# Performance work log

Measured on AMD Instinct MI355X. Metric: run time of the kernel, lower is better.

Reference implementation:

```python
import jax, jax.numpy as jnp
import numpy as np

N = 100000
D_FEAT = 256
HID = 128
EMB = 64
FANOUT = 16


def setup_inputs() -> dict:
    key = jax.random.key(0)
    k = jax.random.split(key, 7)
    s = 0.05
    features = jax.random.normal(k[0], (N, D_FEAT), dtype=jnp.float32)
    W1 = jax.random.normal(k[1], (HID, 2 * D_FEAT), dtype=jnp.float32) * s
    W2 = jax.random.normal(k[2], (HID, 2 * HID), dtype=jnp.float32) * s
    W3 = jax.random.normal(k[3], (HID, 2 * HID), dtype=jnp.float32) * s
    W4 = jax.random.normal(k[4], (EMB, 2 * HID), dtype=jnp.float32) * s
    nodes = jnp.arange(N, dtype=jnp.int32)
    neigh = jax.random.randint(k[5], (N, FANOUT), 0, N, dtype=jnp.int32)
    return {"features": features, "W1": W1, "W2": W2, "W3": W3, "W4": W4,
            "nodes": nodes, "neigh": neigh}


def _sage_layer(h, neigh, W):
    # MeanAggregator: mean of sampled neighbor features  [N, d]
    neigh_mean = jnp.mean(h[neigh], axis=1)
    # Encoder (gcn=False): relu(W @ cat([self, neigh_mean]).T) -> [N, out]
    combined = jnp.concatenate([h, neigh_mean], axis=1)  # [N, 2d]
    return jax.nn.relu(combined @ W.T)


def reference(features, W1, W2, W3, W4, nodes, neigh):
    h1 = _sage_layer(features, neigh, W1)  # [N, HID]
    h2 = _sage_layer(h1, neigh, W2)        # [N, HID]
    h3 = _sage_layer(h2, neigh, W3)        # [N, HID]
    h4 = _sage_layer(h3, neigh, W4)        # [N, EMB]
    # GraphEmbeddingModule.forward returns gSAGE4(n).t() -> [len(n), EMB]
    return h4[nodes]
```

## Files before the change

### kernel.cpp

```cpp
#include <hip/hip_runtime.h>
#include <hip/hip_bf16.h>


constexpr int N_NODES = 100000;
constexpr int FANOUT  = 16;

typedef __attribute__((ext_vector_type(8))) short short8;
typedef __attribute__((ext_vector_type(4))) float f32x4;

__device__ inline unsigned short bf16_rne(float f) {
    unsigned u = __float_as_uint(f);
    return (unsigned short)((u + 0x7fffu + ((u >> 16) & 1u)) >> 16);
}
__device__ inline float bf16_tof(unsigned short s) {
    return __uint_as_float(((unsigned)s) << 16);
}

__global__ __launch_bounds__(256)
void prep_Bck(const float* __restrict__ W, unsigned short* __restrict__ Bhi,
              unsigned short* __restrict__ Blo, int D_IN, int D_OUT)
{
    int i = blockIdx.x * 256 + threadIdx.x;
    int total = 2 * D_OUT * D_IN;
    if (i >= total) return;
    int c = i / D_IN, k = i % D_IN;
    float v = (c < D_OUT) ? W[(size_t)c * (2 * D_IN) + k]
                          : W[(size_t)(c - D_OUT) * (2 * D_IN) + D_IN + k];
    unsigned short hi = bf16_rne(v);
    Bhi[i] = hi;
    Blo[i] = bf16_rne(v - bf16_tof(hi));
}

__global__ __launch_bounds__(256, 4)
void gemm1(const float* __restrict__ hf,
           const unsigned short* __restrict__ Bhi,
           const unsigned short* __restrict__ Blo,
           float* __restrict__ gs, unsigned short* __restrict__ gn, int N)
{
    constexpr int K = 256, DO = 128, LDA = 40;
    __shared__ unsigned short Ah[64 * LDA], Al[64 * LDA];

    const int tid  = threadIdx.x;
    const int wave = tid >> 6;
    const int lane = tid & 63;
    const int ml   = lane & 15;
    const int quad = lane >> 4;
    const int node0 = blockIdx.x * 64;

    f32x4 acc[4][4];
    #pragma unroll
    for (int mi = 0; mi < 4; ++mi)
        #pragma unroll
        for (int ni = 0; ni < 4; ++ni)
            acc[mi][ni] = (f32x4){0.f, 0.f, 0.f, 0.f};

    for (int k0 = 0; k0 < K; k0 += 32) {
        #pragma unroll
        for (int t = 0; t < 2; ++t) {
            int idx = tid + t * 256;
            int row = idx >> 3, c4 = idx & 7;
            int nd = node0 + row; if (nd >= N) nd = N - 1;
            float4 v = *(const float4*)&hf[(size_t)nd * K + k0 + c4 * 4];
            float vv[4] = {v.x, v.y, v.z, v.w};
            unsigned short hi[4], lo[4];
            #pragma unroll
            for (int e = 0; e < 4; ++e) {
                hi[e] = bf16_rne(vv[e]);
                lo[e] = bf16_rne(vv[e] - bf16_tof(hi[e]));
            }
            *(uint2*)&Ah[row * LDA + c4 * 4] = *(const uint2*)hi;
            *(uint2*)&Al[row * LDA + c4 * 4] = *(const uint2*)lo;
        }
        __syncthreads();

        short8 afh[4], afl[4];
        #pragma unroll
        for (int mi = 0; mi < 4; ++mi) {
            int r = mi * 16 + ml;
            afh[mi] = *(const short8*)&Ah[r * LDA + quad * 8];
            afl[mi] = *(const short8*)&Al[r * LDA + quad * 8];
        }
        #pragma unroll
        for (int ni = 0; ni < 4; ++ni) {
            int c = wave * 64 + ni * 16 + ml;
            short8 bh = *(const short8*)&Bhi[(size_t)c * K + k0 + quad * 8];
            short8 bl = *(const short8*)&Blo[(size_t)c * K + k0 + quad * 8];
            #pragma unroll
            for (int mi = 0; mi < 4; ++mi) {
                acc[mi][ni] = __builtin_amdgcn_mfma_f32_16x16x32_bf16(afl[mi], bh, acc[mi][ni], 0, 0, 0);
                acc[mi][ni] = __builtin_amdgcn_mfma_f32_16x16x32_bf16(afh[mi], bl, acc[mi][ni], 0, 0, 0);
                acc[mi][ni] = __builtin_amdgcn_mfma_f32_16x16x32_bf16(afh[mi], bh, acc[mi][ni], 0, 0, 0);
            }
        }
        __syncthreads();
    }

    #pragma unroll
    for (int mi = 0; mi < 4; ++mi)
        #pragma unroll
        for (int r = 0; r < 4; ++r) {
            int node = node0 + mi * 16 + quad * 4 + r;
            if (node >= N) continue;
            #pragma unroll
            for (int ni = 0; ni < 4; ++ni) {
                int c = wave * 64 + ni * 16 + ml;
                float v = acc[mi][ni][r];
                if (c < DO) gs[(size_t)node * DO + c] = v;
                else        gn[(size_t)node * DO + (c - DO)] = bf16_rne(v);
            }
        }
}

template<int C>
__global__ __launch_bounds__(256, 4)
void fused_layer(const float* __restrict__ gs_in,
                 const unsigned short* __restrict__ gn_in,
                 const int* __restrict__ neigh,
                 const unsigned short* __restrict__ Bhi,
                 const unsigned short* __restrict__ Blo,
                 float* __restrict__ gs_out,
                 unsigned short* __restrict__ gn_out, int N)
{
    constexpr int K = 128, DO = C / 2, NI = C / 64, LDAF = 136;
    __shared__ unsigned short Afh[64 * LDAF], Afl[64 * LDAF];

    const int tid  = threadIdx.x;
    const int wave = tid >> 6;
    const int lane = tid & 63;
    const int ml   = lane & 15;
    const int quad = lane >> 4;
    const int node0 = blockIdx.x * 64;

    {
        const int row = tid >> 2;
        const int seg = tid & 3;
        int nd = node0 + row; if (nd >= N) nd = N - 1;
        const int4* nb4 = (const int4*)(neigh + (size_t)nd * FANOUT);
        int4 q0 = nb4[0], q1 = nb4[1], q2 = nb4[2], q3 = nb4[3];
        int ids[FANOUT] = {q0.x, q0.y, q0.z, q0.w, q1.x, q1.y, q1.z, q1.w,
                           q2.x, q2.y, q2.z, q2.w, q3.x, q3.y, q3.z, q3.w};
        float acc[32];
        #pragma unroll
        for (int c = 0; c < 32; ++c) acc[c] = 0.f;
        #pragma unroll
        for (int j = 0; j < FANOUT; ++j) {
            const uint4* src = (const uint4*)&gn_in[(size_t)ids[j] * 128 + seg * 32];
            #pragma unroll
            for (int t = 0; t < 4; ++t) {
                uint4 q = src[t];
                acc[t*8+0] += __uint_as_float(q.x << 16);
                acc[t*8+1] += __uint_as_float(q.x & 0xffff0000u);
                acc[t*8+2] += __uint_as_float(q.y << 16);
                acc[t*8+3] += __uint_as_float(q.y & 0xffff0000u);
                acc[t*8+4] += __uint_as_float(q.z << 16);
                acc[t*8+5] += __uint_as_float(q.z & 0xffff0000u);
                acc[t*8+6] += __uint_as_float(q.w << 16);
                acc[t*8+7] += __uint_as_float(q.w & 0xffff0000u);
            }
        }
        const float inv = 1.0f / (float)FANOUT;
        alignas(16) unsigned short th[32], tl[32];
        const float4* gsp = (const float4*)&gs_in[(size_t)nd * 128 + seg * 32];
        #pragma unroll
        for (int t = 0; t < 8; ++t) {
            float4 s = gsp[t];
            float sv[4] = {s.x, s.y, s.z, s.w};
            #pragma unroll
            for (int e = 0; e < 4; ++e) {
                float h = fmaxf(fmaf(acc[t*4+e], inv, sv[e]), 0.f);
                unsigned short hi = bf16_rne(h);
                th[t*4+e] = hi;
                tl[t*4+e] = bf16_rne(h - bf16_tof(hi));
            }
        }
        #pragma unroll
        for (int t = 0; t < 4; ++t) {
            *(uint4*)&Afh[row * LDAF + seg * 32 + t * 8] = *(const uint4*)&th[t * 8];
            *(uint4*)&Afl[row * LDAF + seg * 32 + t * 8] = *(const uint4*)&tl[t * 8];
        }
    }
    __syncthreads();

    f32x4 acc[4][NI];
    #pragma unroll
    for (int mi = 0; mi < 4; ++mi)
        #pragma unroll
        for (int ni = 0; ni < NI; ++ni)
            acc[mi][ni] = (f32x4){0.f, 0.f, 0.f, 0.f};

    for (int k0 = 0; k0 < K; k0 += 32) {
        short8 afh[4], afl[4];
        #pragma unroll
        for (int mi = 0; mi < 4; ++mi) {
            int r = mi * 16 + ml;
            afh[mi] = *(const short8*)&Afh[r * LDAF + k0 + quad * 8];
            afl[mi] = *(const short8*)&Afl[r * LDAF + k0 + quad * 8];
        }
        #pragma unroll
        for (int ni = 0; ni < NI; ++ni) {
            int c = wave * (16 * NI) + ni * 16 + ml;
            short8 bh = *(const short8*)&Bhi[(size_t)c * K + k0 + quad * 8];
            short8 bl = *(const short8*)&Blo[(size_t)c * K + k0 + quad * 8];
            #pragma unroll
            for (int mi = 0; mi < 4; ++mi) {
                acc[mi][ni] = __builtin_amdgcn_mfma_f32_16x16x32_bf16(afl[mi], bh, acc[mi][ni], 0, 0, 0);
                acc[mi][ni] = __builtin_amdgcn_mfma_f32_16x16x32_bf16(afh[mi], bl, acc[mi][ni], 0, 0, 0);
                acc[mi][ni] = __builtin_amdgcn_mfma_f32_16x16x32_bf16(afh[mi], bh, acc[mi][ni], 0, 0, 0);
            }
        }
    }

    #pragma unroll
    for (int mi = 0; mi < 4; ++mi)
        #pragma unroll
        for (int r = 0; r < 4; ++r) {
            int node = node0 + mi * 16 + quad * 4 + r;
            if (node >= N) continue;
            #pragma unroll
            for (int ni = 0; ni < NI; ++ni) {
                int c = wave * (16 * NI) + ni * 16 + ml;
                float v = acc[mi][ni][r];
                if (c < DO) gs_out[(size_t)node * DO + c] = v;
                else        gn_out[(size_t)node * DO + (c - DO)] = bf16_rne(v);
            }
        }
}

__global__ __launch_bounds__(256)
void agg_out(const float* __restrict__ gs4, const unsigned short* __restrict__ gn4,
             const int* __restrict__ neigh, const int* __restrict__ nodes,
             float* __restrict__ out, int N)
{
    const int i    = blockIdx.x * 32 + (threadIdx.x >> 3);
    const int lane = threadIdx.x & 7;
    if (i >= N) return;
    const int nd = nodes[i];
    const int4* nb4 = (const int4*)(neigh + (size_t)nd * FANOUT);
    int4 q0 = nb4[0], q1 = nb4[1], q2 = nb4[2], q3 = nb4[3];
    int ids[FANOUT] = {q0.x, q0.y, q0.z, q0.w, q1.x, q1.y, q1.z, q1.w,
                       q2.x, q2.y, q2.z, q2.w, q3.x, q3.y, q3.z, q3.w};
    float acc[8];
    #pragma unroll
    for (int c = 0; c < 8; ++c) acc[c] = 0.f;
    #pragma unroll
    for (int j = 0; j < FANOUT; ++j) {
        uint4 q = *(const uint4*)&gn4[(size_t)ids[j] * 64 + lane * 8];
        acc[0] += __uint_as_float(q.x << 16);
        acc[1] += __uint_as_float(q.x & 0xffff0000u);
        acc[2] += __uint_as_float(q.y << 16);
        acc[3] += __uint_as_float(q.y & 0xffff0000u);
        acc[4] += __uint_as_float(q.z << 16);
        acc[5] += __uint_as_float(q.z & 0xffff0000u);
        acc[6] += __uint_as_float(q.w << 16);
        acc[7] += __uint_as_float(q.w & 0xffff0000u);
    }
    const float inv = 1.0f / (float)FANOUT;
    const float* s = gs4 + (size_t)nd * 64 + lane * 8;
    float4 s0 = *(const float4*)&s[0];
    float4 s1 = *(const float4*)&s[4];
    float4 o0, o1;
    o0.x = fmaxf(fmaf(acc[0], inv, s0.x), 0.f);
    o0.y = fmaxf(fmaf(acc[1], inv, s0.y), 0.f);
    o0.z = fmaxf(fmaf(acc[2], inv, s0.z), 0.f);
    o0.w = fmaxf(fmaf(acc[3], inv, s0.w), 0.f);
    o1.x = fmaxf(fmaf(acc[4], inv, s1.x), 0.f);
    o1.y = fmaxf(fmaf(acc[5], inv, s1.y), 0.f);
    o1.z = fmaxf(fmaf(acc[6], inv, s1.z), 0.f);
    o1.w = fmaxf(fmaf(acc[7], inv, s1.w), 0.f);
    float* op = out + (size_t)i * 64 + lane * 8;
    *(float4*)&op[0] = o0;
    *(float4*)&op[4] = o1;
}

extern "C" void kernel_launch(void* const* d_in, const int* in_sizes, int n_in,
                              void* d_out, int out_size, void* d_ws, size_t ws_size,
                              hipStream_t stream)
{
    const float* features = (const float*)d_in[0];
    const float* W1       = (const float*)d_in[1];
    const float* W2       = (const float*)d_in[2];
    const float* W3       = (const float*)d_in[3];
    const float* W4       = (const float*)d_in[4];
    const int*   nodes    = (const int*)d_in[5];
    const int*   neigh    = (const int*)d_in[6];
    float*       out      = (float*)d_out;

    unsigned short* B1h = (unsigned short*)d_ws;
    unsigned short* B1l = B1h + 65536;
    unsigned short* B2h = B1l + 65536;
    unsigned short* B2l = B2h + 32768;
    unsigned short* B3h = B2l + 32768;
    unsigned short* B3l = B3h + 32768;
    unsigned short* B4h = B3l + 32768;
    unsigned short* B4l = B4h + 16384;
    float* gs = (float*)(B4l + 16384);
    unsigned short* gnA = (unsigned short*)(gs + (size_t)N_NODES * 128);
    unsigned short* gnB = gnA + (size_t)N_NODES * 128;
    float* gs4 = (float*)gnB;
    unsigned short* gn4 = gnB + (size_t)N_NODES * 128;

    prep_Bck<<<(65536 + 255) / 256, 256, 0, stream>>>(W1, B1h, B1l, 256, 128);
    prep_Bck<<<(32768 + 255) / 256, 256, 0, stream>>>(W2, B2h, B2l, 128, 128);
    prep_Bck<<<(32768 + 255) / 256, 256, 0, stream>>>(W3, B3h, B3l, 128, 128);
    prep_Bck<<<(16384 + 255) / 256, 256, 0, stream>>>(W4, B4h, B4l, 128, 64);

    const int grid = (N_NODES + 63) / 64;

    gemm1<<<grid, 256, 0, stream>>>(features, B1h, B1l, gs, gnA, N_NODES);
    fused_layer<256><<<grid, 256, 0, stream>>>(gs, gnA, neigh, B2h, B2l, gs, gnB, N_NODES);
    fused_layer<256><<<grid, 256, 0, stream>>>(gs, gnB, neigh, B3h, B3l, gs, gnA, N_NODES);
    fused_layer<128><<<grid, 256, 0, stream>>>(gs, gnA, neigh, B4h, B4l, gs4, gn4, N_NODES);
    agg_out<<<(N_NODES + 31) / 32, 256, 0, stream>>>(gs4, gn4, neigh, nodes, out, N_NODES);
}
```

Baseline: 537.6 us.

## Pre-swizzle weight fragments for coalesced MFMA loads and prefetch gemm1 A tiles

The weight-prep kernel now writes the hi/lo bf16 split weights in an MFMA-fragment-major layout, so each wave's B fragment load is one contiguous 1KB read indexed by lane instead of strided row reads. gemm1 also register-prefetches the next K-slice of fp32 features while the current slice is converted and consumed, overlapping global latency with compute. The launch-bounds occupancy hint for gemm1 drops from 4 to 3 to leave room for the extra prefetch registers, which may lower occupancy.

```diff
diff --git a/kernel.cpp b/kernel.cpp
--- a/kernel.cpp
+++ b/kernel.cpp
@@ -17,21 +17,25 @@
 }
 
 __global__ __launch_bounds__(256)
-void prep_Bck(const float* __restrict__ W, unsigned short* __restrict__ Bhi,
+void prep_Bsw(const float* __restrict__ W, unsigned short* __restrict__ Bhi,
               unsigned short* __restrict__ Blo, int D_IN, int D_OUT)
 {
     int i = blockIdx.x * 256 + threadIdx.x;
     int total = 2 * D_OUT * D_IN;
     if (i >= total) return;
-    int c = i / D_IN, k = i % D_IN;
-    float v = (c < D_OUT) ? W[(size_t)c * (2 * D_IN) + k]
-                          : W[(size_t)(c - D_OUT) * (2 * D_IN) + D_IN + k];
+    int K = D_IN, C = 2 * D_OUT;
+    int c = i / K, k = i % K;
+    float v = (c < D_OUT) ? W[(size_t)c * (2 * K) + k]
+                          : W[(size_t)(c - D_OUT) * (2 * K) + K + k];
+    int tc = c >> 4, mlc = c & 15;
+    int tk = k >> 5, qk = (k >> 3) & 3, e = k & 7;
+    size_t off = ((size_t)(tk * (C / 16) + tc) * 64 + qk * 16 + mlc) * 8 + e;
     unsigned short hi = bf16_rne(v);
-    Bhi[i] = hi;
-    Blo[i] = bf16_rne(v - bf16_tof(hi));
-}
-
-__global__ __launch_bounds__(256, 4)
+    Bhi[off] = hi;
+    Blo[off] = bf16_rne(v - bf16_tof(hi));
+}
+
+__global__ __launch_bounds__(256, 3)
 void gemm1(const float* __restrict__ hf,
            const unsigned short* __restrict__ Bhi,
            const unsigned short* __restrict__ Blo,
@@ -47,6 +51,13 @@
     const int quad = lane >> 4;
     const int node0 = blockIdx.x * 64;
 
+    const int srow = tid >> 3;
+    const int sc4  = tid & 7;
+    int nd0 = node0 + srow;      if (nd0 >= N) nd0 = N - 1;
+    int nd1 = node0 + srow + 32; if (nd1 >= N) nd1 = N - 1;
+    const float* pA0 = &hf[(size_t)nd0 * K + sc4 * 4];
+    const float* pA1 = &hf[(size_t)nd1 * K + sc4 * 4];
+
     f32x4 acc[4][4];
     #pragma unroll
     for (int mi = 0; mi < 4; ++mi)
@@ -54,22 +65,27 @@
         for (int ni = 0; ni < 4; ++ni)
             acc[mi][ni] = (f32x4){0.f, 0.f, 0.f, 0.f};
 
+    float4 pf0 = *(const float4*)&pA0[0];
+    float4 pf1 = *(const float4*)&pA1[0];
+
     for (int k0 = 0; k0 < K; k0 += 32) {
-        #pragma unroll
-        for (int t = 0; t < 2; ++t) {
-            int idx = tid + t * 256;
-            int row = idx >> 3, c4 = idx & 7;
-            int nd = node0 + row; if (nd >= N) nd = N - 1;
-            float4 v = *(const float4*)&hf[(size_t)nd * K + k0 + c4 * 4];
-            float vv[4] = {v.x, v.y, v.z, v.w};
-            unsigned short hi[4], lo[4];
+        {
+            float v0[4] = {pf0.x, pf0.y, pf0.z, pf0.w};
+            float v1[4] = {pf1.x, pf1.y, pf1.z, pf1.w};
+            unsigned short h0[4], l0[4], h1[4], l1[4];
             #pragma unroll
             for (int e = 0; e < 4; ++e) {
-                hi[e] = bf16_rne(vv[e]);
-                lo[e] = bf16_rne(vv[e] - bf16_tof(hi[e]));
-            }
-            *(uint2*)&Ah[row * LDA + c4 * 4] = *(const uint2*)hi;
-            *(uint2*)&Al[row * LDA + c4 * 4] = *(const uint2*)lo;
+                h0[e] = bf16_rne(v0[e]); l0[e] = bf16_rne(v0[e] - bf16_tof(h0[e]));
+                h1[e] = bf16_rne(v1[e]); l1[e] = bf16_rne(v1[e] - bf16_tof(h1[e]));
+            }
+            *(uint2*)&Ah[srow * LDA + sc4 * 4]        = *(const uint2*)h0;
+            *(uint2*)&Al[srow * LDA + sc4 * 4]        = *(const uint2*)l0;
+            *(uint2*)&Ah[(srow + 32) * LDA + sc4 * 4] = *(const uint2*)h1;
+            *(uint2*)&Al[(srow + 32) * LDA + sc4 * 4] = *(const uint2*)l1;
+        }
+        if (k0 + 32 < K) {
+            pf0 = *(const float4*)&pA0[k0 + 32];
+            pf1 = *(const float4*)&pA1[k0 + 32];
         }
         __syncthreads();
 
@@ -80,11 +96,11 @@
             afh[mi] = *(const short8*)&Ah[r * LDA + quad * 8];
             afl[mi] = *(const short8*)&Al[r * LDA + quad * 8];
         }
+        const size_t bbase = (size_t)((k0 >> 5) * 16 + wave * 4) * 512 + (size_t)lane * 8;
         #pragma unroll
         for (int ni = 0; ni < 4; ++ni) {
-            int c = wave * 64 + ni * 16 + ml;
-            short8 bh = *(const short8*)&Bhi[(size_t)c * K + k0 + quad * 8];
-            short8 bl = *(const short8*)&Blo[(size_t)c * K + k0 + quad * 8];
+            short8 bh = *(const short8*)&Bhi[bbase + ni * 512];
+            short8 bl = *(const short8*)&Blo[bbase + ni * 512];
             #pragma unroll
             for (int mi = 0; mi < 4; ++mi) {
                 acc[mi][ni] = __builtin_amdgcn_mfma_f32_16x16x32_bf16(afl[mi], bh, acc[mi][ni], 0, 0, 0);
@@ -196,11 +212,11 @@
             afh[mi] = *(const short8*)&Afh[r * LDAF + k0 + quad * 8];
             afl[mi] = *(const short8*)&Afl[r * LDAF + k0 + quad * 8];
         }
+        const size_t bbase = (size_t)((k0 >> 5) * (C / 16) + wave * NI) * 512 + (size_t)lane * 8;
         #pragma unroll
         for (int ni = 0; ni < NI; ++ni) {
-            int c = wave * (16 * NI) + ni * 16 + ml;
-            short8 bh = *(const short8*)&Bhi[(size_t)c * K + k0 + quad * 8];
-            short8 bl = *(const short8*)&Blo[(size_t)c * K + k0 + quad * 8];
+            short8 bh = *(const short8*)&Bhi[bbase + ni * 512];
+            short8 bl = *(const short8*)&Blo[bbase + ni * 512];
             #pragma unroll
             for (int mi = 0; mi < 4; ++mi) {
                 acc[mi][ni] = __builtin_amdgcn_mfma_f32_16x16x32_bf16(afl[mi], bh, acc[mi][ni], 0, 0, 0);
@@ -299,10 +315,10 @@
     float* gs4 = (float*)gnB;
     unsigned short* gn4 = gnB + (size_t)N_NODES * 128;
 
-    prep_Bck<<<(65536 + 255) / 256, 256, 0, stream>>>(W1, B1h, B1l, 256, 128);
-    prep_Bck<<<(32768 + 255) / 256, 256, 0, stream>>>(W2, B2h, B2l, 128, 128);
-    prep_Bck<<<(32768 + 255) / 256, 256, 0, stream>>>(W3, B3h, B3l, 128, 128);
-    prep_Bck<<<(16384 + 255) / 256, 256, 0, stream>>>(W4, B4h, B4l, 128, 64);
+    prep_Bsw<<<(65536 + 255) / 256, 256, 0, stream>>>(W1, B1h, B1l, 256, 128);
+    prep_Bsw<<<(32768 + 255) / 256, 256, 0, stream>>>(W2, B2h, B2l, 128, 128);
+    prep_Bsw<<<(32768 + 255) / 256, 256, 0, stream>>>(W3, B3h, B3l, 128, 128);
+    prep_Bsw<<<(16384 + 255) / 256, 256, 0, stream>>>(W4, B4h, B4l, 128, 64);
 
     const int grid = (N_NODES + 63) / 64;
 
```

After: 488.2 us. -9.2%, faster.
